# Kernel optimization log

Measured on AMD Instinct MI355X. Metric: run time of the kernel, lower is better.

## Reference

```python
import jax, jax.numpy as jnp
import numpy as np
from jax import lax

B, NS, H, L, STEPS, VOCAB, E, DOC = 8, 80, 256, 2, 8, 30000, 128, 16
NN = NS + 1


def _lstm_stack(Wx, Wh, b, carry, x):
    # flax StackedRNNCell of LSTMCells: gate order i,f,g,o; input dense (no bias) + recurrent dense (bias)
    # Wx, Wh: [L, H, 4H]; b: [L, 4H]; carry: (c, h) each [L, ..., H]; x: [..., H]
    c, h = carry
    new_c, new_h = [], []
    inp = x
    for l in range(Wx.shape[0]):
        g = inp @ Wx[l] + h[l] @ Wh[l] + b[l]
        i, f, gg, o = jnp.split(g, 4, axis=-1)
        cl = jax.nn.sigmoid(f) * c[l] + jax.nn.sigmoid(i) * jnp.tanh(gg)
        hl = jax.nn.sigmoid(o) * jnp.tanh(cl)
        new_c.append(cl)
        new_h.append(hl)
        inp = hl
    return (jnp.stack(new_c), jnp.stack(new_h)), inp


def _concat_carry(c, h):
    # tree_leaves order of [(c0,h0),(c1,h1)] is [c0,h0,c1,h1]
    parts = []
    for l in range(c.shape[0]):
        parts += [c[l], h[l]]
    return jnp.concatenate(parts, axis=-1)


def _unconcat_carry(cat, nl):
    leaves = jnp.split(cat, 2 * nl, axis=-1)
    return jnp.stack(leaves[0::2]), jnp.stack(leaves[1::2])


def _ln(x, scale, bias, eps=1e-6):
    mu = x.mean(-1, keepdims=True)
    var = ((x - mu) ** 2).mean(-1, keepdims=True)
    return (x - mu) * lax.rsqrt(var + eps) * scale + bias


def _skip_encoder(se_nh, Wx, Wh, b, ln_s, ln_b):
    # skip_emb[i, j] = LayerNormed stacked-LSTM run over statements i..j-1; shape [NN, NN, H]
    ns, hd = se_nh.shape
    nl = Wx.shape[0]
    zc = jnp.zeros((nl, hd), se_nh.dtype)

    def from_start(start):
        def f(carry, xt):
            (c, h), idx = carry
            (c2, h2), out = _lstm_stack(Wx, Wh, b, (c, h), xt)
            c2, h2 = _unconcat_carry(_ln(_concat_carry(c2, h2), ln_s, ln_b), nl)
            keep = idx >= start
            c2 = jnp.where(keep, c2, zc)
            h2 = jnp.where(keep, h2, zc)
            out = jnp.where(keep, out, jnp.zeros_like(out))
            return ((c2, h2), idx + 1), out

        _, outs = lax.scan(f, ((zc, zc), 0), se_nh)
        return jnp.concatenate([jnp.zeros((1, hd), se_nh.dtype), outs], axis=0)

    return jax.vmap(from_start)(jnp.arange(ns + 1))


def _forward(node_embeddings, st_Wx, st_Wh, st_b, sk_Wx, sk_Wh, sk_b,
             ln_scale, ln_bias, ex_Wx, ex_Wh, ex_b, wk, bk, ws, bs,
             w1, b1, wo, bo, exit_node_indexes):
    bsz, ns, hd = node_embeddings.shape
    nl = st_Wx.shape[0]
    nn_ = ns + 1
    # statement embedder: single-token (L=1) stacked-LSTM step from zero state
    z = jnp.zeros((nl, bsz, ns, hd), node_embeddings.dtype)
    _, stmt = _lstm_stack(st_Wx, st_Wh, st_b, (z, z), node_embeddings)  # [B, NS, H]
    skip = jax.vmap(lambda s: _skip_encoder(s, sk_Wx, sk_Wh, sk_b, ln_scale, ln_bias))(stmt)  # [B, NN, NN, H]
    keys = jnp.einsum('bnmh,hk->bnmk', skip, ws) + bs  # skip_dense, reused every step
    c = jnp.zeros((nl, bsz, nn_, hd), node_embeddings.dtype)
    h = jnp.zeros_like(c)
    p = jnp.zeros((bsz, nn_), node_embeddings.dtype).at[:, 0].set(1.0)
    mask_mid = (1.0 - jnp.tri(nn_)).at[:, ns].set(1.0)
    mask_init = jnp.zeros((nn_, nn_)).at[:, 1].set(1.0)
    mask_fin = jnp.zeros((nn_, nn_)).at[:, ns].set(1.0)
    for step_idx in range(STEPS):
        mask = mask_init if step_idx == 0 else (mask_fin if step_idx == STEPS - 1 else mask_mid)
        hcat = _concat_carry(c, h)  # [B, NN, 2*L*H]
        q = hcat @ wk + bk  # h_key dense -> [B, NN, H]
        logits = (jnp.tanh(q[:, :, None, :] + keys) @ w1)[..., 0] + b1[0]  # [B, NN, NN]
        logits = jnp.where(mask > 0, logits, -1e9)
        a = jax.nn.softmax(logits, axis=-1)
        t = p[:, :, None] * a  # transition mass [B, NN, NN]
        new_p = t.sum(axis=1)
        denom = new_p[:, :, None] + 1e-7
        x_in = jnp.einsum('bnm,bnmh->bmh', t, skip) / denom
        c_prop = jnp.einsum('bnm,lbnh->lbmh', t, c) / denom[None]
        h_prop = jnp.einsum('bnm,lbnh->lbmh', t, h) / denom[None]
        (c, h), _ = _lstm_stack(ex_Wx, ex_Wh, ex_b, (c_prop, h_prop), x_in)
        p = new_p
    h_exit = h[-1][jnp.arange(bsz), exit_node_indexes]  # [B, H]
    return h_exit @ wo + bo  # [B, VOCAB]


def setup_inputs():
    key = jax.random.key(0)
    ks = jax.random.split(key, 20)
    s = 1.0 / np.sqrt(H)

    def nrm(k, shape, scale):
        return jax.random.normal(k, shape, dtype=jnp.float32) * scale

    return dict(
        node_embeddings=nrm(ks[0], (B, NS, H), 1.0),
        docstring_embeddings=nrm(ks[1], (B, DOC, H), 1.0),
        docstring_mask=jnp.ones((B, DOC), dtype=bool),
        edge_sources=jax.random.randint(ks[2], (B, E), 0, NN, dtype=jnp.int32),
        edge_dests=jax.random.randint(ks[3], (B, E), 0, NN, dtype=jnp.int32),
        edge_types=jax.random.randint(ks[4], (B, E), 0, 6, dtype=jnp.int32),
        true_indexes=jax.random.randint(ks[5], (B, NS), 0, NN, dtype=jnp.int32),
        false_indexes=jax.random.randint(ks[6], (B, NS), 0, NN, dtype=jnp.int32),
        raise_indexes=jax.random.randint(ks[7], (B, NS), 0, NN, dtype=jnp.int32),
        start_node_indexes=jnp.zeros((B,), dtype=jnp.int32),
        exit_node_indexes=jnp.full((B,), NS, dtype=jnp.int32),
        step_limits=jnp.full((B,), STEPS, dtype=jnp.int32),
        st_Wx=nrm(ks[8], (L, H, 4 * H), s), st_Wh=nrm(ks[9], (L, H, 4 * H), s),
        st_b=jnp.zeros((L, 4 * H)),
        sk_Wx=nrm(ks[10], (L, H, 4 * H), s), sk_Wh=nrm(ks[11], (L, H, 4 * H), s),
        sk_b=jnp.zeros((L, 4 * H)),
        ln_scale=jnp.ones((2 * L * H,)), ln_bias=jnp.zeros((2 * L * H,)),
        ex_Wx=nrm(ks[12], (L, H, 4 * H), s), ex_Wh=nrm(ks[13], (L, H, 4 * H), s),
        ex_b=jnp.zeros((L, 4 * H)),
        wk=nrm(ks[14], (2 * L * H, H), 1.0 / np.sqrt(2 * L * H)), bk=jnp.zeros((H,)),
        ws=nrm(ks[15], (H, H), s), bs=jnp.zeros((H,)),
        w1=nrm(ks[16], (H, 1), s), b1=jnp.zeros((1,)),
        wo=nrm(ks[17], (H, VOCAB), s), bo=jnp.zeros((VOCAB,)),
    )


def reference(node_embeddings, docstring_embeddings, docstring_mask, edge_sources,
              edge_dests, edge_types, true_indexes, false_indexes, raise_indexes,
              start_node_indexes, exit_node_indexes, step_limits,
              st_Wx, st_Wh, st_b, sk_Wx, sk_Wh, sk_b, ln_scale, ln_bias,
              ex_Wx, ex_Wh, ex_b, wk, bk, ws, bs, w1, b1, wo, bo):
    # docstring_* and edge index args are accepted per the model signature but are
    # not used in the visible forward body.
    return _forward(node_embeddings, st_Wx, st_Wh, st_b, sk_Wx, sk_Wh, sk_b,
                    ln_scale, ln_bias, ex_Wx, ex_Wh, ex_b, wk, bk, ws, bs,
                    w1, b1, wo, bo, exit_node_indexes)
```

## Files before the change

kernel.cpp:

```cpp
#include <hip/hip_runtime.h>

typedef unsigned int  u32;
typedef unsigned short u16;
typedef float v2f __attribute__((ext_vector_type(2)));
typedef __attribute__((ext_vector_type(8))) short bfv8;
typedef __attribute__((ext_vector_type(4))) float f32x4;

#define ROWS 648

__device__ __forceinline__ float sigf(float x){ return 1.0f/(1.0f+__expf(-x)); }
__device__ __forceinline__ float tanh_fast(float x){
  float e = __expf(-2.0f*fabsf(x));
  float r = (1.0f-e)/(1.0f+e);
  return copysignf(r,x);
}
__device__ __forceinline__ u16 f2bf(float f){
  u32 u = __float_as_uint(f);
  u += 0x7FFFu + ((u>>16)&1u);
  return (u16)(u>>16);
}
__device__ __forceinline__ u32 packbf2(float lo, float hi){
  return (u32)f2bf(lo) | ((u32)f2bf(hi)<<16);
}
__device__ __forceinline__ float bf2f(u16 v){ return __uint_as_float(((u32)v)<<16); }
__device__ __forceinline__ float bflo(u32 u){ return __uint_as_float(u<<16); }
__device__ __forceinline__ float bfhi(u32 u){ return __uint_as_float(u & 0xFFFF0000u); }
__device__ __forceinline__ v2f unpk(u32 w){
  v2f r; r.x = bflo(w); r.y = bfhi(w); return r;
}

__global__ void pack_pairs(const float* __restrict__ src, u32* __restrict__ dst,
                           int Kpairs, int ncol){
  int id = blockIdx.x*256 + threadIdx.x;
  if (id >= Kpairs*ncol) return;
  int k2 = id / ncol, j = id - k2*ncol;
  dst[id] = packbf2(src[(2*k2)*ncol + j], src[(2*k2+1)*ncol + j]);
}

__global__ void pack_mfma(const float* __restrict__ A, const float* __restrict__ Bm,
                          u32* __restrict__ dst, int K){
  int id = blockIdx.x*256 + threadIdx.x;
  int KS = K >> 5;
  int tot = 64*KS*64*4;
  if (id >= tot) return;
  int e2 = id & 3;
  int l  = (id >> 2) & 63;
  int rest = id >> 8;
  int ks = rest % KS;
  int t  = rest / KS;
  int k  = ks*32 + (l>>4)*8 + e2*2;
  int col = t*16 + (l&15);
  float v0 = (k   < 256) ? A[k*1024 + col]       : Bm[(k-256)*1024 + col];
  float v1 = (k+1 < 256) ? A[(k+1)*1024 + col]   : Bm[(k+1-256)*1024 + col];
  dst[id] = packbf2(v0, v1);
}

__global__ void k_init_p(float* __restrict__ p0){
  int i = blockIdx.x*256 + threadIdx.x;
  if (i < ROWS) p0[i] = ((i % 81)==0) ? 1.0f : 0.0f;
}

__global__ __launch_bounds__(512) void k_stmt_x0(
    const float* __restrict__ ne, const float* __restrict__ stWx, const float* __restrict__ stb,
    const float* __restrict__ skWx, const float* __restrict__ skb, float4* __restrict__ X0){
  __shared__ float xv[2][256];
  __shared__ float hv[2][256];
  int r = threadIdx.x >> 8, j = threadIdx.x & 255;
  int bn = blockIdx.x*2 + r;
  xv[r][j] = ne[bn*256 + j];
  __syncthreads();
  float a0=stb[j], a2=stb[512+j], a3=stb[768+j];
  for (int k=0;k<256;k++){
    float x = xv[r][k];
    const float* w = stWx + k*1024;
    a0 = fmaf(x, w[j], a0); a2 = fmaf(x, w[512+j], a2); a3 = fmaf(x, w[768+j], a3);
  }
  float c = sigf(a0)*tanh_fast(a2);
  float h = sigf(a3)*tanh_fast(c);
  hv[r][j] = h;
  __syncthreads();
  a0=stb[1024+j]; a2=stb[1536+j]; a3=stb[1792+j];
  const float* W1 = stWx + 256*1024;
  for (int k=0;k<256;k++){
    float x = hv[r][k];
    const float* w = W1 + k*1024;
    a0 = fmaf(x, w[j], a0); a2 = fmaf(x, w[512+j], a2); a3 = fmaf(x, w[768+j], a3);
  }
  c = sigf(a0)*tanh_fast(a2);
  h = sigf(a3)*tanh_fast(c);
  __syncthreads();
  xv[r][j] = h;
  __syncthreads();
  float b0=skb[j], b1g=skb[256+j], b2=skb[512+j], b3=skb[768+j];
  for (int k=0;k<256;k++){
    float x = xv[r][k];
    const float* w = skWx + k*1024;
    b0 = fmaf(x, w[j], b0);     b1g = fmaf(x, w[256+j], b1g);
    b2 = fmaf(x, w[512+j], b2); b3 = fmaf(x, w[768+j], b3);
  }
  X0[bn*256 + j] = make_float4(b0,b1g,b2,b3);
}

#define RS0 264
#define RS1 520
__global__ __launch_bounds__(1024) void k_skip_chains(
    const float4* __restrict__ X0,
    const uint4* __restrict__ W0m, const uint4* __restrict__ W1m,
    const float* __restrict__ skb, const float* __restrict__ lnS, const float* __restrict__ lnB,
    float* __restrict__ skip){
  int s  = blockIdx.x;
  int tid = threadIdx.x;
  int w = tid >> 6, lane = tid & 63;
  int l15 = lane & 15, l4 = lane >> 4;
  int rp = tid >> 8, j = tid & 255;
  __shared__ float part[8*1024];
  __shared__ u16 A0h[16*RS0], A0l[16*RS0];
  __shared__ u16 A1h[16*RS1], A1l[16*RS1];
  __shared__ float red[4][16];
  for (int i=tid; i<16*RS0; i+=1024){ A0h[i]=0; A0l[i]=0; }
  for (int i=tid; i<16*RS1; i+=1024){ A1h[i]=0; A1l[i]=0; }
  float c0a=0.f, c1a=0.f, c0b=0.f, c1b=0.f;
  float s1b0=skb[1024+j], s1b1=skb[1280+j], s1b2=skb[1536+j], s1b3=skb[1792+j];
  float lS0=lnS[j], lS1=lnS[256+j], lS2=lnS[512+j], lS3=lnS[768+j];
  float lB0=lnB[j], lB1=lnB[256+j], lB2=lnB[512+j], lB3=lnB[768+j];
  const int aoff0 = l15*RS0 + l4*8;
  const int aoff1 = l15*RS1 + l4*8;
  __syncthreads();
  for (int idx=s; idx<80; idx++){
    float4 gxa = X0[(rp*80+idx)*256 + j];
    float4 gxb = X0[((rp+4)*80+idx)*256 + j];
    f32x4 acc0={0,0,0,0}, acc1={0,0,0,0}, acc2={0,0,0,0}, acc3={0,0,0,0};
    #pragma unroll 4
    for (int ks=0; ks<8; ks++){
      bfv8 ah = *(const bfv8*)&A0h[aoff0 + ks*32];
      bfv8 al = *(const bfv8*)&A0l[aoff0 + ks*32];
      uint4 b0 = W0m[((w*4+0)*8 + ks)*64 + lane];
      uint4 b1 = W0m[((w*4+1)*8 + ks)*64 + lane];
      uint4 b2 = W0m[((w*4+2)*8 + ks)*64 + lane];
      uint4 b3 = W0m[((w*4+3)*8 + ks)*64 + lane];
      bfv8 v0=__builtin_bit_cast(bfv8,b0), v1=__builtin_bit_cast(bfv8,b1);
      bfv8 v2=__builtin_bit_cast(bfv8,b2), v3=__builtin_bit_cast(bfv8,b3);
      acc0=__builtin_amdgcn_mfma_f32_16x16x32_bf16(ah,v0,acc0,0,0,0);
      acc0=__builtin_amdgcn_mfma_f32_16x16x32_bf16(al,v0,acc0,0,0,0);
      acc1=__builtin_amdgcn_mfma_f32_16x16x32_bf16(ah,v1,acc1,0,0,0);
      acc1=__builtin_amdgcn_mfma_f32_16x16x32_bf16(al,v1,acc1,0,0,0);
      acc2=__builtin_amdgcn_mfma_f32_16x16x32_bf16(ah,v2,acc2,0,0,0);
      acc2=__builtin_amdgcn_mfma_f32_16x16x32_bf16(al,v2,acc2,0,0,0);
      acc3=__builtin_amdgcn_mfma_f32_16x16x32_bf16(ah,v3,acc3,0,0,0);
      acc3=__builtin_amdgcn_mfma_f32_16x16x32_bf16(al,v3,acc3,0,0,0);
    }
    if (lane < 32){
      int r0 = l4*4;
      #pragma unroll
      for (int q=0;q<4;q++){
        part[(r0+q)*1024 + w*64 +  0 + l15] = acc0[q];
        part[(r0+q)*1024 + w*64 + 16 + l15] = acc1[q];
        part[(r0+q)*1024 + w*64 + 32 + l15] = acc2[q];
        part[(r0+q)*1024 + w*64 + 48 + l15] = acc3[q];
      }
    }
    __syncthreads();
    float h0na, h0nb;
    {
      float a0=gxa.x+part[rp*1024+j],     a1=gxa.y+part[rp*1024+256+j];
      float a2=gxa.z+part[rp*1024+512+j], a3=gxa.w+part[rp*1024+768+j];
      float ii=sigf(a0), ff=sigf(a1), gg=tanh_fast(a2), oo=sigf(a3);
      c0a = ff*c0a + ii*gg;
      h0na = oo*tanh_fast(c0a);
      u16 hi = f2bf(h0na);
      A1h[rp*RS1 + j] = hi;
      A1l[rp*RS1 + j] = f2bf(h0na - bf2f(hi));
    }
    {
      int rb = rp+4;
      float a0=gxb.x+part[rb*1024+j],     a1=gxb.y+part[rb*1024+256+j];
      float a2=gxb.z+part[rb*1024+512+j], a3=gxb.w+part[rb*1024+768+j];
      float ii=sigf(a0), ff=sigf(a1), gg=tanh_fast(a2), oo=sigf(a3);
      c0b = ff*c0b + ii*gg;
      h0nb = oo*tanh_fast(c0b);
      u16 hi = f2bf(h0nb);
      A1h[rb*RS1 + j] = hi;
      A1l[rb*RS1 + j] = f2bf(h0nb - bf2f(hi));
    }
    __syncthreads();
    acc0=(f32x4){0,0,0,0}; acc1=(f32x4){0,0,0,0}; acc2=(f32x4){0,0,0,0}; acc3=(f32x4){0,0,0,0};
    #pragma unroll 4
    for (int ks=0; ks<16; ks++){
      bfv8 ah = *(const bfv8*)&A1h[aoff1 + ks*32];
      bfv8 al = *(const bfv8*)&A1l[aoff1 + ks*32];
      uint4 b0 = W1m[((w*4+0)*16 + ks)*64 + lane];
      uint4 b1 = W1m[((w*4+1)*16 + ks)*64 + lane];
      uint4 b2 = W1m[((w*4+2)*16 + ks)*64 + lane];
      uint4 b3 = W1m[((w*4+3)*16 + ks)*64 + lane];
      bfv8 v0=__builtin_bit_cast(bfv8,b0), v1=__builtin_bit_cast(bfv8,b1);
      bfv8 v2=__builtin_bit_cast(bfv8,b2), v3=__builtin_bit_cast(bfv8,b3);
      acc0=__builtin_amdgcn_mfma_f32_16x16x32_bf16(ah,v0,acc0,0,0,0);
      acc0=__builtin_amdgcn_mfma_f32_16x16x32_bf16(al,v0,acc0,0,0,0);
      acc1=__builtin_amdgcn_mfma_f32_16x16x32_bf16(ah,v1,acc1,0,0,0);
      acc1=__builtin_amdgcn_mfma_f32_16x16x32_bf16(al,v1,acc1,0,0,0);
      acc2=__builtin_amdgcn_mfma_f32_16x16x32_bf16(ah,v2,acc2,0,0,0);
      acc2=__builtin_amdgcn_mfma_f32_16x16x32_bf16(al,v2,acc2,0,0,0);
      acc3=__builtin_amdgcn_mfma_f32_16x16x32_bf16(ah,v3,acc3,0,0,0);
      acc3=__builtin_amdgcn_mfma_f32_16x16x32_bf16(al,v3,acc3,0,0,0);
    }
    if (lane < 32){
      int r0 = l4*4;
      #pragma unroll
      for (int q=0;q<4;q++){
        part[(r0+q)*1024 + w*64 +  0 + l15] = acc0[q];
        part[(r0+q)*1024 + w*64 + 16 + l15] = acc1[q];
        part[(r0+q)*1024 + w*64 + 32 + l15] = acc2[q];
        part[(r0+q)*1024 + w*64 + 48 + l15] = acc3[q];
      }
    }
    __syncthreads();
    float h1na, h1nb;
    {
      float a0=s1b0+part[rp*1024+j],     a1=s1b1+part[rp*1024+256+j];
      float a2=s1b2+part[rp*1024+512+j], a3=s1b3+part[rp*1024+768+j];
      float ii=sigf(a0), ff=sigf(a1), gg=tanh_fast(a2), oo=sigf(a3);
      c1a = ff*c1a + ii*gg;
      h1na = oo*tanh_fast(c1a);
      skip[((rp*81 + s)*81 + (idx+1))*256 + j] = h1na;
    }
    {
      int rb = rp+4;
      float a0=s1b0+part[rb*1024+j],     a1=s1b1+part[rb*1024+256+j];
      float a2=s1b2+part[rb*1024+512+j], a3=s1b3+part[rb*1024+768+j];
      float ii=sigf(a0), ff=sigf(a1), gg=tanh_fast(a2), oo=sigf(a3);
      c1b = ff*c1b + ii*gg;
      h1nb = oo*tanh_fast(c1b);
      skip[((rb*81 + s)*81 + (idx+1))*256 + j] = h1nb;
    }
    float sm0 = c0a + h0na + c1a + h1na;
    float sq0 = c0a*c0a + h0na*h0na + c1a*c1a + h1na*h1na;
    float sm1 = c0b + h0nb + c1b + h1nb;
    float sq1 = c0b*c0b + h0nb*h0nb + c1b*c1b + h1nb*h1nb;
    #pragma unroll
    for (int off=32; off; off>>=1){
      sm0 += __shfl_xor(sm0, off); sq0 += __shfl_xor(sq0, off);
      sm1 += __shfl_xor(sm1, off); sq1 += __shfl_xor(sq1, off);
    }
    int wq = j >> 6;
    if ((j & 63) == 0){
      red[rp][wq*4+0]=sm0; red[rp][wq*4+1]=sq0;
      red[rp][wq*4+2]=sm1; red[rp][wq*4+3]=sq1;
    }
    __syncthreads();
    sm0 = red[rp][0]+red[rp][4]+red[rp][8]+red[rp][12];
    sq0 = red[rp][1]+red[rp][5]+red[rp][9]+red[rp][13];
    sm1 = red[rp][2]+red[rp][6]+red[rp][10]+red[rp][14];
    sq1 = red[rp][3]+red[rp][7]+red[rp][11]+red[rp][15];
    {
      float mu = sm0 * (1.0f/1024.0f);
      float var = sq0 * (1.0f/1024.0f) - mu*mu;
      float rstd = rsqrtf(var + 1e-6f);
      c0a = (c0a - mu)*rstd*lS0 + lB0;
      float h0ln = (h0na - mu)*rstd*lS1 + lB1;
      c1a = (c1a - mu)*rstd*lS2 + lB2;
      float h1ln = (h1na - mu)*rstd*lS3 + lB3;
      u16 hi = f2bf(h0ln);
      A0h[rp*RS0 + j] = hi; A0l[rp*RS0 + j] = f2bf(h0ln - bf2f(hi));
      hi = f2bf(h1ln);
      A1h[rp*RS1 + 256 + j] = hi; A1l[rp*RS1 + 256 + j] = f2bf(h1ln - bf2f(hi));
    }
    {
      int rb = rp+4;
      float mu = sm1 * (1.0f/1024.0f);
      float var = sq1 * (1.0f/1024.0f) - mu*mu;
      float rstd = rsqrtf(var + 1e-6f);
      c0b = (c0b - mu)*rstd*lS0 + lB0;
      float h0ln = (h0nb - mu)*rstd*lS1 + lB1;
      c1b = (c1b - mu)*rstd*lS2 + lB2;
      float h1ln = (h1nb - mu)*rstd*lS3 + lB3;
      u16 hi = f2bf(h0ln);
      A0h[rb*RS0 + j] = hi; A0l[rb*RS0 + j] = f2bf(h0ln - bf2f(hi));
      hi = f2bf(h1ln);
      A1h[rb*RS1 + 256 + j] = hi; A1l[rb*RS1 + 256 + j] = f2bf(h1ln - bf2f(hi));
    }
    __syncthreads();
  }
}

__global__ __launch_bounds__(256) void k_keys(const float* __restrict__ skip,
    const u32* __restrict__ wspk, const float* __restrict__ bs, u16* __restrict__ keys){
  __shared__ float skr[8][256];
  int tid = threadIdx.x;
  int bn = blockIdx.x;
  float bsv = bs[tid];
  const float4* sk4 = (const float4*)skip;
  for (int m0=0; m0<81; m0+=8){
    int mc = (81-m0 < 8) ? (81-m0) : 8;
    for (int i=tid; i<mc*64; i+=256){
      int mm = i>>6, kk = i&63;
      float4 v = sk4[(bn*81 + m0 + mm)*64 + kk];
      skr[mm][4*kk+0]=v.x; skr[mm][4*kk+1]=v.y; skr[mm][4*kk+2]=v.z; skr[mm][4*kk+3]=v.w;
    }
    __syncthreads();
    v2f acc[8];
    #pragma unroll
    for (int qq=0;qq<8;qq++) acc[qq]=(v2f){0.f,0.f};
    for (int k2=0;k2<128;k2++){
      v2f w2 = unpk(wspk[k2*256+tid]);
      #pragma unroll
      for (int qq=0;qq<8;qq++){
        v2f sv = *(const v2f*)&skr[qq][2*k2];
        acc[qq] += sv*w2;
      }
    }
    for (int qq=0;qq<mc;qq++) keys[(bn*81+m0+qq)*256+tid] = f2bf(acc[qq].x+acc[qq].y+bsv);
    __syncthreads();
  }
}

__global__ __launch_bounds__(256) void k_attn(
    const float* __restrict__ c0g, const float* __restrict__ h0g,
    const float* __restrict__ c1g, const float* __restrict__ h1g,
    const u32* __restrict__ wkp, const float* __restrict__ bk,
    const u16* __restrict__ keys, const float* __restrict__ w1,
    const float* __restrict__ pcur, float* __restrict__ t, int mode){
  int bn = blockIdx.x; int n = bn % 81;
  int tid = threadIdx.x;
  float pv = pcur[bn];
  if (pv == 0.0f){
    if (tid < 81) t[bn*81 + tid] = 0.0f;
    return;
  }
  __shared__ float hc[1024];
  __shared__ float qv[256];
  __shared__ float lg[81];
  hc[tid]      = c0g[bn*256+tid];
  hc[256+tid]  = h0g[bn*256+tid];
  hc[512+tid]  = c1g[bn*256+tid];
  hc[768+tid]  = h1g[bn*256+tid];
  if (tid < 81) lg[tid] = -3e38f;
  __syncthreads();
  v2f A = {bk[tid], 0.f};
  #pragma unroll 8
  for (int k2=0;k2<512;k2++){
    v2f hp = *(const v2f*)&hc[2*k2];
    A += hp*unpk(wkp[k2*256+tid]);
  }
  qv[tid] = A.x + A.y;
  __syncthreads();
  int lane = tid & 63, wv = tid >> 6;
  float w1v0 = w1[lane], w1v1 = w1[64+lane], w1v2 = w1[128+lane], w1v3 = w1[192+lane];
  for (int m = wv; m < 81; m += 4){
    bool um = (mode==0) ? (m==1) : (mode==2) ? (m==80) : (m>n || m==80);
    if (!um) continue;
    const u16* kr = keys + (bn*81+m)*256;
    float acc;
    acc  = tanh_fast(qv[lane]     + bf2f(kr[lane]))     * w1v0;
    acc += tanh_fast(qv[64+lane]  + bf2f(kr[64+lane]))  * w1v1;
    acc += tanh_fast(qv[128+lane] + bf2f(kr[128+lane])) * w1v2;
    acc += tanh_fast(qv[192+lane] + bf2f(kr[192+lane])) * w1v3;
    #pragma unroll
    for (int off=32; off; off>>=1) acc += __shfl_xor(acc, off);
    if (lane==0) lg[m] = acc;
  }
  __syncthreads();
  if (tid < 64){
    float v1 = lg[tid];
    float v2 = (tid<17) ? lg[64+tid] : -3e38f;
    float mx = fmaxf(v1, v2);
    #pragma unroll
    for (int off=32; off; off>>=1) mx = fmaxf(mx, __shfl_xor(mx, off));
    float e1 = __expf(v1-mx);
    float e2 = (tid<17) ? __expf(v2-mx) : 0.0f;
    float ssum = e1+e2;
    #pragma unroll
    for (int off=32; off; off>>=1) ssum += __shfl_xor(ssum, off);
    float sc = pv / ssum;
    t[bn*81 + tid] = e1*sc;
    if (tid<17) t[bn*81 + 64+tid] = e2*sc;
  }
}

__global__ __launch_bounds__(256) void k_gather(
    const float* __restrict__ t, const float* __restrict__ skip,
    const float* __restrict__ c0i, const float* __restrict__ h0i,
    const float* __restrict__ c1i, const float* __restrict__ h1i,
    float* __restrict__ xin, float* __restrict__ h0p,
    float* __restrict__ h1p, float* __restrict__ c0p,
    float* __restrict__ c1p, float* __restrict__ pnext){
  int row = blockIdx.x;
  int b = row / 81, m = row - b*81;
  int tid = threadIdx.x;
  __shared__ float tcol[81];
  if (tid < 81) tcol[tid] = t[(b*81+tid)*81 + m];
  __syncthreads();
  int nlim = (m==80) ? 81 : m;
  float ts = 0.f;
  for (int n=0;n<nlim;n++) ts += tcol[n];
  if (tid==0) pnext[row] = ts;
  int o = row*256 + tid;
  if (ts == 0.0f){
    xin[o]=0.f; h0p[o]=0.f; h1p[o]=0.f; c0p[o]=0.f; c1p[o]=0.f;
    return;
  }
  float xa=0.f, c0a=0.f, h0a=0.f, c1a=0.f, h1a=0.f;
  for (int n=0;n<nlim;n++){
    float tv = tcol[n];
    int st = (b*81+n)*256 + tid;
    xa  = fmaf(tv, skip[((b*81+n)*81 + m)*256 + tid], xa);
    c0a = fmaf(tv, c0i[st], c0a);
    h0a = fmaf(tv, h0i[st], h0a);
    c1a = fmaf(tv, c1i[st], c1a);
    h1a = fmaf(tv, h1i[st], h1a);
  }
  float inv = 1.0f/(ts + 1e-7f);
  xin[o]=xa*inv; h0p[o]=h0a*inv; h1p[o]=h1a*inv; c0p[o]=c0a*inv; c1p[o]=c1a*inv;
}

#define RSX 520
__global__ __launch_bounds__(1024) void k_exlstm(
    const float* __restrict__ xin, const float* __restrict__ h0pg,
    const float* __restrict__ h1pg, const float* __restrict__ c0pg,
    const float* __restrict__ c1pg,
    const uint4* __restrict__ WAm, const uint4* __restrict__ WBm,
    const float* __restrict__ exb,
    float* __restrict__ c0o, float* __restrict__ h0o,
    float* __restrict__ c1o, float* __restrict__ h1o){
  int row0 = blockIdx.x*16;
  int tid = threadIdx.x;
  int w = tid >> 6, lane = tid & 63;
  int l15 = lane & 15, l4 = lane >> 4;
  int rp = tid >> 8, j = tid & 255;
  __shared__ float part[16*1024];
  __shared__ u16 Ah[16*RSX], Al[16*RSX];
  {
    int r16 = w, c4 = lane;
    int grow = row0 + r16;
    float4 vx = {0,0,0,0}, vh = {0,0,0,0};
    if (grow < ROWS){
      vx = ((const float4*)xin)[grow*64 + c4];
      vh = ((const float4*)h0pg)[grow*64 + c4];
    }
    ushort4 hi4, lo4;
    hi4.x=f2bf(vx.x); lo4.x=f2bf(vx.x-bf2f(hi4.x));
    hi4.y=f2bf(vx.y); lo4.y=f2bf(vx.y-bf2f(hi4.y));
    hi4.z=f2bf(vx.z); lo4.z=f2bf(vx.z-bf2f(hi4.z));
    hi4.w=f2bf(vx.w); lo4.w=f2bf(vx.w-bf2f(hi4.w));
    *(ushort4*)&Ah[r16*RSX + c4*4] = hi4;
    *(ushort4*)&Al[r16*RSX + c4*4] = lo4;
    hi4.x=f2bf(vh.x); lo4.x=f2bf(vh.x-bf2f(hi4.x));
    hi4.y=f2bf(vh.y); lo4.y=f2bf(vh.y-bf2f(hi4.y));
    hi4.z=f2bf(vh.z); lo4.z=f2bf(vh.z-bf2f(hi4.z));
    hi4.w=f2bf(vh.w); lo4.w=f2bf(vh.w-bf2f(hi4.w));
    *(ushort4*)&Ah[r16*RSX + 256 + c4*4] = hi4;
    *(ushort4*)&Al[r16*RSX + 256 + c4*4] = lo4;
  }
  __syncthreads();
  const int aoff = l15*RSX + l4*8;
  f32x4 acc0={0,0,0,0}, acc1={0,0,0,0}, acc2={0,0,0,0}, acc3={0,0,0,0};
  #pragma unroll 4
  for (int ks=0; ks<16; ks++){
    bfv8 ah = *(const bfv8*)&Ah[aoff + ks*32];
    bfv8 al = *(const bfv8*)&Al[aoff + ks*32];
    uint4 b0 = WAm[((w*4+0)*16 + ks)*64 + lane];
    uint4 b1 = WAm[((w*4+1)*16 + ks)*64 + lane];
    uint4 b2 = WAm[((w*4+2)*16 + ks)*64 + lane];
    uint4 b3 = WAm[((w*4+3)*16 + ks)*64 + lane];
    bfv8 v0=__builtin_bit_cast(bfv8,b0), v1=__builtin_bit_cast(bfv8,b1);
    bfv8 v2=__builtin_bit_cast(bfv8,b2), v3=__builtin_bit_cast(bfv8,b3);
    acc0=__builtin_amdgcn_mfma_f32_16x16x32_bf16(ah,v0,acc0,0,0,0);
    acc0=__builtin_amdgcn_mfma_f32_16x16x32_bf16(al,v0,acc0,0,0,0);
    acc1=__builtin_amdgcn_mfma_f32_16x16x32_bf16(ah,v1,acc1,0,0,0);
    acc1=__builtin_amdgcn_mfma_f32_16x16x32_bf16(al,v1,acc1,0,0,0);
    acc2=__builtin_amdgcn_mfma_f32_16x16x32_bf16(ah,v2,acc2,0,0,0);
    acc2=__builtin_amdgcn_mfma_f32_16x16x32_bf16(al,v2,acc2,0,0,0);
    acc3=__builtin_amdgcn_mfma_f32_16x16x32_bf16(ah,v3,acc3,0,0,0);
    acc3=__builtin_amdgcn_mfma_f32_16x16x32_bf16(al,v3,acc3,0,0,0);
  }
  {
    int r0 = l4*4;
    #pragma unroll
    for (int q=0;q<4;q++){
      part[(r0+q)*1024 + w*64 +  0 + l15] = acc0[q];
      part[(r0+q)*1024 + w*64 + 16 + l15] = acc1[q];
      part[(r0+q)*1024 + w*64 + 32 + l15] = acc2[q];
      part[(r0+q)*1024 + w*64 + 48 + l15] = acc3[q];
    }
  }
  __syncthreads();
  float eb0=exb[j], eb1=exb[256+j], eb2=exb[512+j], eb3=exb[768+j];
  float c0s[4], h0s[4];
  #pragma unroll
  for (int q=0;q<4;q++){
    int r = 4*q + rp;
    int grow = row0 + r;
    bool g = grow < ROWS;
    float a0 = eb0 + part[r*1024 + j];
    float a1 = eb1 + part[r*1024 + 256 + j];
    float a2 = eb2 + part[r*1024 + 512 + j];
    float a3 = eb3 + part[r*1024 + 768 + j];
    float cp = g ? c0pg[grow*256 + j] : 0.f;
    float ii=sigf(a0), ff=sigf(a1), gg=tanh_fast(a2), oo=sigf(a3);
    float cn = ff*cp + ii*gg;
    float hn = oo*tanh_fast(cn);
    c0s[q]=cn; h0s[q]=hn;
    u16 hi = f2bf(hn);
    Ah[r*RSX + j] = hi; Al[r*RSX + j] = f2bf(hn - bf2f(hi));
    float hp = g ? h1pg[grow*256 + j] : 0.f;
    hi = f2bf(hp);
    Ah[r*RSX + 256 + j] = hi; Al[r*RSX + 256 + j] = f2bf(hp - bf2f(hi));
  }
  __syncthreads();
  acc0=(f32x4){0,0,0,0}; acc1=(f32x4){0,0,0,0}; acc2=(f32x4){0,0,0,0}; acc3=(f32x4){0,0,0,0};
  #pragma unroll 4
  for (int ks=0; ks<16; ks++){
    bfv8 ah = *(const bfv8*)&Ah[aoff + ks*32];
    bfv8 al = *(const bfv8*)&Al[aoff + ks*32];
    uint4 b0 = WBm[((w*4+0)*16 + ks)*64 + lane];
    uint4 b1 = WBm[((w*4+1)*16 + ks)*64 + lane];
    uint4 b2 = WBm[((w*4+2)*16 + ks)*64 + lane];
    uint4 b3 = WBm[((w*4+3)*16 + ks)*64 + lane];
    bfv8 v0=__builtin_bit_cast(bfv8,b0), v1=__builtin_bit_cast(bfv8,b1);
    bfv8 v2=__builtin_bit_cast(bfv8,b2), v3=__builtin_bit_cast(bfv8,b3);
    acc0=__builtin_amdgcn_mfma_f32_16x16x32_bf16(ah,v0,acc0,0,0,0);
    acc0=__builtin_amdgcn_mfma_f32_16x16x32_bf16(al,v0,acc0,0,0,0);
    acc1=__builtin_amdgcn_mfma_f32_16x16x32_bf16(ah,v1,acc1,0,0,0);
    acc1=__builtin_amdgcn_mfma_f32_16x16x32_bf16(al,v1,acc1,0,0,0);
    acc2=__builtin_amdgcn_mfma_f32_16x16x32_bf16(ah,v2,acc2,0,0,0);
    acc2=__builtin_amdgcn_mfma_f32_16x16x32_bf16(al,v2,acc2,0,0,0);
    acc3=__builtin_amdgcn_mfma_f32_16x16x32_bf16(ah,v3,acc3,0,0,0);
    acc3=__builtin_amdgcn_mfma_f32_16x16x32_bf16(al,v3,acc3,0,0,0);
  }
  {
    int r0 = l4*4;
    #pragma unroll
    for (int q=0;q<4;q++){
      part[(r0+q)*1024 + w*64 +  0 + l15] = acc0[q];
      part[(r0+q)*1024 + w*64 + 16 + l15] = acc1[q];
      part[(r0+q)*1024 + w*64 + 32 + l15] = acc2[q];
      part[(r0+q)*1024 + w*64 + 48 + l15] = acc3[q];
    }
  }
  __syncthreads();
  float eb4=exb[1024+j], eb5=exb[1280+j], eb6=exb[1536+j], eb7=exb[1792+j];
  #pragma unroll
  for (int q=0;q<4;q++){
    int r = 4*q + rp;
    int grow = row0 + r;
    bool g = grow < ROWS;
    float a0 = eb4 + part[r*1024 + j];
    float a1 = eb5 + part[r*1024 + 256 + j];
    float a2 = eb6 + part[r*1024 + 512 + j];
    float a3 = eb7 + part[r*1024 + 768 + j];
    float cp = g ? c1pg[grow*256 + j] : 0.f;
    float ii=sigf(a0), ff=sigf(a1), gg=tanh_fast(a2), oo=sigf(a3);
    float cn = ff*cp + ii*gg;
    float hn = oo*tanh_fast(cn);
    if (g){
      int o = grow*256 + j;
      c0o[o]=c0s[q]; h0o[o]=h0s[q]; c1o[o]=cn; h1o[o]=hn;
    }
  }
}

__global__ __launch_bounds__(256) void k_out(
    const float* __restrict__ h1f, const int* __restrict__ exitIdx,
    const float* __restrict__ wo, const float* __restrict__ bo, float* __restrict__ out){
  __shared__ float hv[8][256];
  int tid = threadIdx.x;
  for (int i = tid; i < 2048; i += 256){
    int b = i >> 8, k = i & 255;
    hv[b][k] = h1f[(b*81 + exitIdx[b])*256 + k];
  }
  __syncthreads();
  int v = blockIdx.x*256 + tid;
  if (v >= 30000) return;
  float acc[8];
  #pragma unroll
  for (int b=0;b<8;b++) acc[b] = bo[v];
  for (int k=0;k<256;k++){
    float w = wo[k*30000 + v];
    #pragma unroll
    for (int b=0;b<8;b++) acc[b] = fmaf(hv[b][k], w, acc[b]);
  }
  #pragma unroll
  for (int b=0;b<8;b++) out[b*30000+v] = acc[b];
}

extern "C" void kernel_launch(void* const* d_in, const int* in_sizes, int n_in,
                              void* d_out, int out_size, void* d_ws, size_t ws_size,
                              hipStream_t stream){
  (void)in_sizes; (void)n_in; (void)out_size;
  const float* ne    = (const float*)d_in[0];
  const int*   exitI = (const int*)d_in[10];
  const float* stWx  = (const float*)d_in[12];
  const float* stb   = (const float*)d_in[14];
  const float* skWx  = (const float*)d_in[15];
  const float* skWh  = (const float*)d_in[16];
  const float* skb   = (const float*)d_in[17];
  const float* lnS   = (const float*)d_in[18];
  const float* lnB   = (const float*)d_in[19];
  const float* exWx  = (const float*)d_in[20];
  const float* exWh  = (const float*)d_in[21];
  const float* exb   = (const float*)d_in[22];
  const float* wk    = (const float*)d_in[23];
  const float* bk    = (const float*)d_in[24];
  const float* wsm   = (const float*)d_in[25];
  const float* bs    = (const float*)d_in[26];
  const float* w1    = (const float*)d_in[27];
  const float* wo    = (const float*)d_in[29];
  const float* bo    = (const float*)d_in[30];
  float* out = (float*)d_out;

  char* w = (char*)d_ws;
  size_t off = 0;
  auto alloc = [&](size_t bytes)->char*{
    char* p = w + off; off += (bytes + 255) & ~size_t(255); return p;
  };
  float4* X0   = (float4*)alloc((size_t)640*256*16);
  u32* W0m     = (u32*)alloc((size_t)131072*4);
  u32* W1m     = (u32*)alloc((size_t)262144*4);
  u32* WAm     = (u32*)alloc((size_t)262144*4);
  u32* WBm     = (u32*)alloc((size_t)262144*4);
  u32* wkp     = (u32*)alloc((size_t)512*256*4);
  u32* wspk    = (u32*)alloc((size_t)128*256*4);
  float* skip  = (float*)alloc((size_t)8*81*81*256*4);
  u16* keys    = (u16*)alloc((size_t)8*81*81*256*2);
  float* tb    = (float*)alloc((size_t)ROWS*81*4);
  float* p0    = (float*)alloc(ROWS*4);
  float* p1    = (float*)alloc(ROWS*4);
  float* stA   = (float*)alloc((size_t)4*ROWS*256*4);
  float* stB   = (float*)alloc((size_t)4*ROWS*256*4);
  float* xinb  = (float*)alloc((size_t)ROWS*256*4);
  float* h0pb  = (float*)alloc((size_t)ROWS*256*4);
  float* h1pb  = (float*)alloc((size_t)ROWS*256*4);
  float* c0pb  = (float*)alloc((size_t)ROWS*256*4);
  float* c1pb  = (float*)alloc((size_t)ROWS*256*4);
  if (off > ws_size) return;

  const size_t ST = (size_t)ROWS*256;
  float *A_c0=stA, *A_h0=stA+ST, *A_c1=stA+2*ST, *A_h1=stA+3*ST;
  float *B_c0=stB, *B_h0=stB+ST, *B_c1=stB+2*ST, *B_h1=stB+3*ST;

  hipMemsetAsync(skip, 0, (size_t)8*81*81*256*4, stream);
  hipMemsetAsync(stA, 0, (size_t)4*ROWS*256*4, stream);
  hipMemsetAsync(stB, 0, (size_t)4*ROWS*256*4, stream);
  k_init_p<<<3,256,0,stream>>>(p0);

  pack_mfma<<<512, 256, 0, stream>>>(skWh, skWh, W0m, 256);
  pack_mfma<<<1024,256, 0, stream>>>(skWx+256*1024, skWh+256*1024, W1m, 512);
  pack_mfma<<<1024,256, 0, stream>>>(exWx, exWh, WAm, 512);
  pack_mfma<<<1024,256, 0, stream>>>(exWx+256*1024, exWh+256*1024, WBm, 512);
  pack_pairs<<<512, 256, 0, stream>>>(wk, wkp, 512, 256);
  pack_pairs<<<128, 256, 0, stream>>>(wsm, wspk, 128, 256);

  k_stmt_x0<<<320, 512, 0, stream>>>(ne, stWx, stb, skWx, skb, X0);
  k_skip_chains<<<80, 1024, 0, stream>>>(X0, (const uint4*)W0m, (const uint4*)W1m,
                                         skb, lnS, lnB, skip);
  k_keys<<<648, 256, 0, stream>>>(skip, wspk, bs, keys);

  float* pc = p0; float* pn = p1;
  for (int s=0; s<8; s++){
    float *ic0,*ih0,*ic1,*ih1,*oc0,*oh0,*oc1,*oh1;
    if ((s & 1) == 0){ ic0=A_c0; ih0=A_h0; ic1=A_c1; ih1=A_h1; oc0=B_c0; oh0=B_h0; oc1=B_c1; oh1=B_h1; }
    else             { ic0=B_c0; ih0=B_h0; ic1=B_c1; ih1=B_h1; oc0=A_c0; oh0=A_h0; oc1=A_c1; oh1=A_h1; }
    int mode = (s==0) ? 0 : ((s==7) ? 2 : 1);
    k_attn<<<648, 256, 0, stream>>>(ic0, ih0, ic1, ih1, wkp, bk, keys, w1, pc, tb, mode);
    k_gather<<<648, 256, 0, stream>>>(tb, skip, ic0, ih0, ic1, ih1,
                                      xinb, h0pb, h1pb, c0pb, c1pb, pn);
    k_exlstm<<<41, 1024, 0, stream>>>(xinb, h0pb, h1pb, c0pb, c1pb,
                                      (const uint4*)WAm, (const uint4*)WBm, exb,
                                      oc0, oh0, oc1, oh1);
    float* tmp = pc; pc = pn; pn = tmp;
  }
  k_out<<<(30000+255)/256, 256, 0, stream>>>(A_h1, exitI, wo, bo, out);
}
```

Measured before the change: 2.267 ms.

## Move key and query projections to split-bf16 MFMA and fuse query into exit LSTM

The skip-embedding key projection changes from a scalar packed-bf16 loop to MFMA tiles of 16 rows, using hi/lo bf16 splitting to keep fp32-like accuracy. The per-step query projection (carry times wk) moves out of k_attn into the tail of k_exlstm, where the new carry is already in registers and can be staged in LDS for MFMA. k_attn now reads the precomputed query, and its mode 0 and mode 2 steps exit early with a one-hot result. Shared partial buffers are padded to reduce LDS bank conflicts. The cost is extra LDS and a third MFMA phase in k_exlstm, which runs on only 41 blocks.

```diff
diff --git a/kernel.cpp b/kernel.cpp
--- a/kernel.cpp
+++ b/kernel.cpp
@@ -7,6 +7,7 @@
 typedef __attribute__((ext_vector_type(4))) float f32x4;
 
 #define ROWS 648
+#define KROWS 52488
 
 __device__ __forceinline__ float sigf(float x){ return 1.0f/(1.0f+__expf(-x)); }
 __device__ __forceinline__ float tanh_fast(float x){
@@ -23,19 +24,6 @@
   return (u32)f2bf(lo) | ((u32)f2bf(hi)<<16);
 }
 __device__ __forceinline__ float bf2f(u16 v){ return __uint_as_float(((u32)v)<<16); }
-__device__ __forceinline__ float bflo(u32 u){ return __uint_as_float(u<<16); }
-__device__ __forceinline__ float bfhi(u32 u){ return __uint_as_float(u & 0xFFFF0000u); }
-__device__ __forceinline__ v2f unpk(u32 w){
-  v2f r; r.x = bflo(w); r.y = bfhi(w); return r;
-}
-
-__global__ void pack_pairs(const float* __restrict__ src, u32* __restrict__ dst,
-                           int Kpairs, int ncol){
-  int id = blockIdx.x*256 + threadIdx.x;
-  if (id >= Kpairs*ncol) return;
-  int k2 = id / ncol, j = id - k2*ncol;
-  dst[id] = packbf2(src[(2*k2)*ncol + j], src[(2*k2+1)*ncol + j]);
-}
 
 __global__ void pack_mfma(const float* __restrict__ A, const float* __restrict__ Bm,
                           u32* __restrict__ dst, int K){
@@ -55,6 +43,23 @@
   dst[id] = packbf2(v0, v1);
 }
 
+__global__ void pack_w(const float* __restrict__ src, u32* __restrict__ dst,
+                       int K, int NT){
+  int id = blockIdx.x*256 + threadIdx.x;
+  int KS = K >> 5;
+  int tot = NT*KS*64*4;
+  if (id >= tot) return;
+  int e2 = id & 3;
+  int l  = (id >> 2) & 63;
+  int rest = id >> 8;
+  int ks = rest % KS;
+  int t  = rest / KS;
+  int k  = ks*32 + (l>>4)*8 + e2*2;
+  int col = t*16 + (l&15);
+  int ld = NT*16;
+  dst[id] = packbf2(src[k*ld + col], src[(k+1)*ld + col]);
+}
+
 __global__ void k_init_p(float* __restrict__ p0){
   int i = blockIdx.x*256 + threadIdx.x;
   if (i < ROWS) p0[i] = ((i % 81)==0) ? 1.0f : 0.0f;
@@ -103,6 +108,7 @@
 
 #define RS0 264
 #define RS1 520
+#define PS  1028
 __global__ __launch_bounds__(1024) void k_skip_chains(
     const float4* __restrict__ X0,
     const uint4* __restrict__ W0m, const uint4* __restrict__ W1m,
@@ -113,7 +119,7 @@
   int w = tid >> 6, lane = tid & 63;
   int l15 = lane & 15, l4 = lane >> 4;
   int rp = tid >> 8, j = tid & 255;
-  __shared__ float part[8*1024];
+  __shared__ float part[8*PS];
   __shared__ u16 A0h[16*RS0], A0l[16*RS0];
   __shared__ u16 A1h[16*RS1], A1l[16*RS1];
   __shared__ float red[4][16];
@@ -153,17 +159,17 @@
       int r0 = l4*4;
       #pragma unroll
       for (int q=0;q<4;q++){
-        part[(r0+q)*1024 + w*64 +  0 + l15] = acc0[q];
-        part[(r0+q)*1024 + w*64 + 16 + l15] = acc1[q];
-        part[(r0+q)*1024 + w*64 + 32 + l15] = acc2[q];
-        part[(r0+q)*1024 + w*64 + 48 + l15] = acc3[q];
+        part[(r0+q)*PS + w*64 +  0 + l15] = acc0[q];
+        part[(r0+q)*PS + w*64 + 16 + l15] = acc1[q];
+        part[(r0+q)*PS + w*64 + 32 + l15] = acc2[q];
+        part[(r0+q)*PS + w*64 + 48 + l15] = acc3[q];
       }
     }
     __syncthreads();
     float h0na, h0nb;
     {
-      float a0=gxa.x+part[rp*1024+j],     a1=gxa.y+part[rp*1024+256+j];
-      float a2=gxa.z+part[rp*1024+512+j], a3=gxa.w+part[rp*1024+768+j];
+      float a0=gxa.x+part[rp*PS+j],     a1=gxa.y+part[rp*PS+256+j];
+      float a2=gxa.z+part[rp*PS+512+j], a3=gxa.w+part[rp*PS+768+j];
       float ii=sigf(a0), ff=sigf(a1), gg=tanh_fast(a2), oo=sigf(a3);
       c0a = ff*c0a + ii*gg;
       h0na = oo*tanh_fast(c0a);
@@ -173,8 +179,8 @@
     }
     {
       int rb = rp+4;
-      float a0=gxb.x+part[rb*1024+j],     a1=gxb.y+part[rb*1024+256+j];
-      float a2=gxb.z+part[rb*1024+512+j], a3=gxb.w+part[rb*1024+768+j];
+      float a0=gxb.x+part[rb*PS+j],     a1=gxb.y+part[rb*PS+256+j];
+      float a2=gxb.z+part[rb*PS+512+j], a3=gxb.w+part[rb*PS+768+j];
       float ii=sigf(a0), ff=sigf(a1), gg=tanh_fast(a2), oo=sigf(a3);
       c0b = ff*c0b + ii*gg;
       h0nb = oo*tanh_fast(c0b);
@@ -207,17 +213,17 @@
       int r0 = l4*4;
       #pragma unroll
       for (int q=0;q<4;q++){
-        part[(r0+q)*1024 + w*64 +  0 + l15] = acc0[q];
-        part[(r0+q)*1024 + w*64 + 16 + l15] = acc1[q];
-        part[(r0+q)*1024 + w*64 + 32 + l15] = acc2[q];
-        part[(r0+q)*1024 + w*64 + 48 + l15] = acc3[q];
+        part[(r0+q)*PS + w*64 +  0 + l15] = acc0[q];
+        part[(r0+q)*PS + w*64 + 16 + l15] = acc1[q];
+        part[(r0+q)*PS + w*64 + 32 + l15] = acc2[q];
+        part[(r0+q)*PS + w*64 + 48 + l15] = acc3[q];
       }
     }
     __syncthreads();
     float h1na, h1nb;
     {
-      float a0=s1b0+part[rp*1024+j],     a1=s1b1+part[rp*1024+256+j];
-      float a2=s1b2+part[rp*1024+512+j], a3=s1b3+part[rp*1024+768+j];
+      float a0=s1b0+part[rp*PS+j],     a1=s1b1+part[rp*PS+256+j];
+      float a2=s1b2+part[rp*PS+512+j], a3=s1b3+part[rp*PS+768+j];
       float ii=sigf(a0), ff=sigf(a1), gg=tanh_fast(a2), oo=sigf(a3);
       c1a = ff*c1a + ii*gg;
       h1na = oo*tanh_fast(c1a);
@@ -225,8 +231,8 @@
     }
     {
       int rb = rp+4;
-      float a0=s1b0+part[rb*1024+j],     a1=s1b1+part[rb*1024+256+j];
-      float a2=s1b2+part[rb*1024+512+j], a3=s1b3+part[rb*1024+768+j];
+      float a0=s1b0+part[rb*PS+j],     a1=s1b1+part[rb*PS+256+j];
+      float a2=s1b2+part[rb*PS+512+j], a3=s1b3+part[rb*PS+768+j];
       float ii=sigf(a0), ff=sigf(a1), gg=tanh_fast(a2), oo=sigf(a3);
       c1b = ff*c1b + ii*gg;
       h1nb = oo*tanh_fast(c1b);
@@ -282,43 +288,54 @@
   }
 }
 
-__global__ __launch_bounds__(256) void k_keys(const float* __restrict__ skip,
-    const u32* __restrict__ wspk, const float* __restrict__ bs, u16* __restrict__ keys){
-  __shared__ float skr[8][256];
+__global__ __launch_bounds__(1024) void k_keys(const float* __restrict__ skip,
+    const uint4* __restrict__ WSm, const float* __restrict__ bs, u16* __restrict__ keys){
+  int rows0 = blockIdx.x*16;
   int tid = threadIdx.x;
-  int bn = blockIdx.x;
-  float bsv = bs[tid];
-  const float4* sk4 = (const float4*)skip;
-  for (int m0=0; m0<81; m0+=8){
-    int mc = (81-m0 < 8) ? (81-m0) : 8;
-    for (int i=tid; i<mc*64; i+=256){
-      int mm = i>>6, kk = i&63;
-      float4 v = sk4[(bn*81 + m0 + mm)*64 + kk];
-      skr[mm][4*kk+0]=v.x; skr[mm][4*kk+1]=v.y; skr[mm][4*kk+2]=v.z; skr[mm][4*kk+3]=v.w;
-    }
-    __syncthreads();
-    v2f acc[8];
-    #pragma unroll
-    for (int qq=0;qq<8;qq++) acc[qq]=(v2f){0.f,0.f};
-    for (int k2=0;k2<128;k2++){
-      v2f w2 = unpk(wspk[k2*256+tid]);
-      #pragma unroll
-      for (int qq=0;qq<8;qq++){
-        v2f sv = *(const v2f*)&skr[qq][2*k2];
-        acc[qq] += sv*w2;
-      }
-    }
-    for (int qq=0;qq<mc;qq++) keys[(bn*81+m0+qq)*256+tid] = f2bf(acc[qq].x+acc[qq].y+bsv);
-    __syncthreads();
-  }
+  int w = tid >> 6, lane = tid & 63;
+  int l15 = lane & 15, l4 = lane >> 4;
+  __shared__ u16 Ah[16*RS0], Al[16*RS0];
+  __shared__ u16 kbuf[16*256];
+  {
+    int grow = rows0 + w;
+    float4 v = {0,0,0,0};
+    if (grow < KROWS) v = ((const float4*)skip)[grow*64 + lane];
+    ushort4 hi4, lo4;
+    hi4.x=f2bf(v.x); lo4.x=f2bf(v.x-bf2f(hi4.x));
+    hi4.y=f2bf(v.y); lo4.y=f2bf(v.y-bf2f(hi4.y));
+    hi4.z=f2bf(v.z); lo4.z=f2bf(v.z-bf2f(hi4.z));
+    hi4.w=f2bf(v.w); lo4.w=f2bf(v.w-bf2f(hi4.w));
+    *(ushort4*)&Ah[w*RS0 + lane*4] = hi4;
+    *(ushort4*)&Al[w*RS0 + lane*4] = lo4;
+  }
+  __syncthreads();
+  const int aoff = l15*RS0 + l4*8;
+  f32x4 acc = {0,0,0,0};
+  #pragma unroll
+  for (int ks=0; ks<8; ks++){
+    bfv8 ah = *(const bfv8*)&Ah[aoff + ks*32];
+    bfv8 al = *(const bfv8*)&Al[aoff + ks*32];
+    uint4 b = WSm[(w*8 + ks)*64 + lane];
+    bfv8 v = __builtin_bit_cast(bfv8, b);
+    acc = __builtin_amdgcn_mfma_f32_16x16x32_bf16(ah, v, acc, 0,0,0);
+    acc = __builtin_amdgcn_mfma_f32_16x16x32_bf16(al, v, acc, 0,0,0);
+  }
+  float bsv = bs[w*16 + l15];
+  #pragma unroll
+  for (int q=0;q<4;q++)
+    kbuf[(l4*4+q)*256 + w*16 + l15] = f2bf(acc[q] + bsv);
+  __syncthreads();
+  int nval = KROWS - rows0; if (nval > 16) nval = 16;
+  int words = nval*128;
+  u32* kout = (u32*)keys + (size_t)rows0*128;
+  const u32* kin = (const u32*)kbuf;
+  for (int i=tid; i<words; i+=1024) kout[i] = kin[i];
 }
 
 __global__ __launch_bounds__(256) void k_attn(
-    const float* __restrict__ c0g, const float* __restrict__ h0g,
-    const float* __restrict__ c1g, const float* __restrict__ h1g,
-    const u32* __restrict__ wkp, const float* __restrict__ bk,
-    const u16* __restrict__ keys, const float* __restrict__ w1,
-    const float* __restrict__ pcur, float* __restrict__ t, int mode){
+    const float* __restrict__ qb, const u16* __restrict__ keys,
+    const float* __restrict__ w1, const float* __restrict__ pcur,
+    float* __restrict__ t, int mode){
   int bn = blockIdx.x; int n = bn % 81;
   int tid = threadIdx.x;
   float pv = pcur[bn];
@@ -326,28 +343,17 @@
     if (tid < 81) t[bn*81 + tid] = 0.0f;
     return;
   }
-  __shared__ float hc[1024];
+  if (mode == 0){ if (tid < 81) t[bn*81 + tid] = (tid==1)  ? pv : 0.0f; return; }
+  if (mode == 2){ if (tid < 81) t[bn*81 + tid] = (tid==80) ? pv : 0.0f; return; }
   __shared__ float qv[256];
   __shared__ float lg[81];
-  hc[tid]      = c0g[bn*256+tid];
-  hc[256+tid]  = h0g[bn*256+tid];
-  hc[512+tid]  = c1g[bn*256+tid];
-  hc[768+tid]  = h1g[bn*256+tid];
+  qv[tid] = qb[bn*256 + tid];
   if (tid < 81) lg[tid] = -3e38f;
-  __syncthreads();
-  v2f A = {bk[tid], 0.f};
-  #pragma unroll 8
-  for (int k2=0;k2<512;k2++){
-    v2f hp = *(const v2f*)&hc[2*k2];
-    A += hp*unpk(wkp[k2*256+tid]);
-  }
-  qv[tid] = A.x + A.y;
   __syncthreads();
   int lane = tid & 63, wv = tid >> 6;
   float w1v0 = w1[lane], w1v1 = w1[64+lane], w1v2 = w1[128+lane], w1v3 = w1[192+lane];
   for (int m = wv; m < 81; m += 4){
-    bool um = (mode==0) ? (m==1) : (mode==2) ? (m==80) : (m>n || m==80);
-    if (!um) continue;
+    if (!(m>n || m==80)) continue;
     const u16* kr = keys + (bn*81+m)*256;
     float acc;
     acc  = tanh_fast(qv[lane]     + bf2f(kr[lane]))     * w1v0;
@@ -412,43 +418,45 @@
   xin[o]=xa*inv; h0p[o]=h0a*inv; h1p[o]=h1a*inv; c0p[o]=c0a*inv; c1p[o]=c1a*inv;
 }
 
-#define RSX 520
+#define RSX 1032
+#define PSX 1028
 __global__ __launch_bounds__(1024) void k_exlstm(
     const float* __restrict__ xin, const float* __restrict__ h0pg,
     const float* __restrict__ h1pg, const float* __restrict__ c0pg,
     const float* __restrict__ c1pg,
     const uint4* __restrict__ WAm, const uint4* __restrict__ WBm,
-    const float* __restrict__ exb,
+    const uint4* __restrict__ WKm,
+    const float* __restrict__ exb, const float* __restrict__ bk,
     float* __restrict__ c0o, float* __restrict__ h0o,
-    float* __restrict__ c1o, float* __restrict__ h1o){
+    float* __restrict__ c1o, float* __restrict__ h1o,
+    float* __restrict__ qb){
   int row0 = blockIdx.x*16;
   int tid = threadIdx.x;
   int w = tid >> 6, lane = tid & 63;
   int l15 = lane & 15, l4 = lane >> 4;
   int rp = tid >> 8, j = tid & 255;
-  __shared__ float part[16*1024];
+  __shared__ float part[16*PSX];
   __shared__ u16 Ah[16*RSX], Al[16*RSX];
   {
-    int r16 = w, c4 = lane;
-    int grow = row0 + r16;
+    int grow = row0 + w;
     float4 vx = {0,0,0,0}, vh = {0,0,0,0};
     if (grow < ROWS){
-      vx = ((const float4*)xin)[grow*64 + c4];
-      vh = ((const float4*)h0pg)[grow*64 + c4];
+      vx = ((const float4*)xin)[grow*64 + lane];
+      vh = ((const float4*)h0pg)[grow*64 + lane];
     }
     ushort4 hi4, lo4;
     hi4.x=f2bf(vx.x); lo4.x=f2bf(vx.x-bf2f(hi4.x));
     hi4.y=f2bf(vx.y); lo4.y=f2bf(vx.y-bf2f(hi4.y));
     hi4.z=f2bf(vx.z); lo4.z=f2bf(vx.z-bf2f(hi4.z));
     hi4.w=f2bf(vx.w); lo4.w=f2bf(vx.w-bf2f(hi4.w));
-    *(ushort4*)&Ah[r16*RSX + c4*4] = hi4;
-    *(ushort4*)&Al[r16*RSX + c4*4] = lo4;
+    *(ushort4*)&Ah[w*RSX + lane*4] = hi4;
+    *(ushort4*)&Al[w*RSX + lane*4] = lo4;
     hi4.x=f2bf(vh.x); lo4.x=f2bf(vh.x-bf2f(hi4.x));
     hi4.y=f2bf(vh.y); lo4.y=f2bf(vh.y-bf2f(hi4.y));
     hi4.z=f2bf(vh.z); lo4.z=f2bf(vh.z-bf2f(hi4.z));
     hi4.w=f2bf(vh.w); lo4.w=f2bf(vh.w-bf2f(hi4.w));
-    *(ushort4*)&Ah[r16*RSX + 256 + c4*4] = hi4;
-    *(ushort4*)&Al[r16*RSX + 256 + c4*4] = lo4;
+    *(ushort4*)&Ah[w*RSX + 256 + lane*4] = hi4;
+    *(ushort4*)&Al[w*RSX + 256 + lane*4] = lo4;
   }
   __syncthreads();
   const int aoff = l15*RSX + l4*8;
@@ -476,10 +484,10 @@
     int r0 = l4*4;
     #pragma unroll
     for (int q=0;q<4;q++){
-      part[(r0+q)*1024 + w*64 +  0 + l15] = acc0[q];
-      part[(r0+q)*1024 + w*64 + 16 + l15] = acc1[q];
-      part[(r0+q)*1024 + w*64 + 32 + l15] = acc2[q];
-      part[(r0+q)*1024 + w*64 + 48 + l15] = acc3[q];
+      part[(r0+q)*PSX + w*64 +  0 + l15] = acc0[q];
+      part[(r0+q)*PSX + w*64 + 16 + l15] = acc1[q];
+      part[(r0+q)*PSX + w*64 + 32 + l15] = acc2[q];
+      part[(r0+q)*PSX + w*64 + 48 + l15] = acc3[q];
     }
   }
   __syncthreads();
@@ -490,10 +498,10 @@
     int r = 4*q + rp;
     int grow = row0 + r;
     bool g = grow < ROWS;
-    float a0 = eb0 + part[r*1024 + j];
-    float a1 = eb1 + part[r*1024 + 256 + j];
-    float a2 = eb2 + part[r*1024 + 512 + j];
-    float a3 = eb3 + part[r*1024 + 768 + j];
+    float a0 = eb0 + part[r*PSX + j];
+    float a1 = eb1 + part[r*PSX + 256 + j];
+    float a2 = eb2 + part[r*PSX + 512 + j];
+    float a3 = eb3 + part[r*PSX + 768 + j];
     float cp = g ? c0pg[grow*256 + j] : 0.f;
     float ii=sigf(a0), ff=sigf(a1), gg=tanh_fast(a2), oo=sigf(a3);
     float cn = ff*cp + ii*gg;
@@ -530,10 +538,10 @@
     int r0 = l4*4;
     #pragma unroll
     for (int q=0;q<4;q++){
-      part[(r0+q)*1024 + w*64 +  0 + l15] = acc0[q];
-      part[(r0+q)*1024 + w*64 + 16 + l15] = acc1[q];
-      part[(r0+q)*1024 + w*64 + 32 + l15] = acc2[q];
-      part[(r0+q)*1024 + w*64 + 48 + l15] = acc3[q];
+      part[(r0+q)*PSX + w*64 +  0 + l15] = acc0[q];
+      part[(r0+q)*PSX + w*64 + 16 + l15] = acc1[q];
+      part[(r0+q)*PSX + w*64 + 32 + l15] = acc2[q];
+      part[(r0+q)*PSX + w*64 + 48 + l15] = acc3[q];
     }
   }
   __syncthreads();
@@ -543,10 +551,10 @@
     int r = 4*q + rp;
     int grow = row0 + r;
     bool g = grow < ROWS;
-    float a0 = eb4 + part[r*1024 + j];
-    float a1 = eb5 + part[r*1024 + 256 + j];
-    float a2 = eb6 + part[r*1024 + 512 + j];
-    float a3 = eb7 + part[r*1024 + 768 + j];
+    float a0 = eb4 + part[r*PSX + j];
+    float a1 = eb5 + part[r*PSX + 256 + j];
+    float a2 = eb6 + part[r*PSX + 512 + j];
+    float a3 = eb7 + part[r*PSX + 768 + j];
     float cp = g ? c1pg[grow*256 + j] : 0.f;
     float ii=sigf(a0), ff=sigf(a1), gg=tanh_fast(a2), oo=sigf(a3);
     float cn = ff*cp + ii*gg;
@@ -555,6 +563,36 @@
       int o = grow*256 + j;
       c0o[o]=c0s[q]; h0o[o]=h0s[q]; c1o[o]=cn; h1o[o]=hn;
     }
+    u16 hi;
+    hi = f2bf(c0s[q]); Ah[r*RSX +       j] = hi; Al[r*RSX +       j] = f2bf(c0s[q]-bf2f(hi));
+    hi = f2bf(h0s[q]); Ah[r*RSX + 256 + j] = hi; Al[r*RSX + 256 + j] = f2bf(h0s[q]-bf2f(hi));
+    hi = f2bf(cn);     Ah[r*RSX + 512 + j] = hi; Al[r*RSX + 512 + j] = f2bf(cn-bf2f(hi));
+    hi = f2bf(hn);     Ah[r*RSX + 768 + j] = hi; Al[r*RSX + 768 + j] = f2bf(hn-bf2f(hi));
+  }
+  __syncthreads();
+  f32x4 accq = {0,0,0,0};
+  #pragma unroll 4
+  for (int ks=0; ks<32; ks++){
+    bfv8 ah = *(const bfv8*)&Ah[aoff + ks*32];
+    bfv8 al = *(const bfv8*)&Al[aoff + ks*32];
+    uint4 b = WKm[(w*32 + ks)*64 + lane];
+    bfv8 v = __builtin_bit_cast(bfv8, b);
+    accq = __builtin_amdgcn_mfma_f32_16x16x32_bf16(ah, v, accq, 0,0,0);
+    accq = __builtin_amdgcn_mfma_f32_16x16x32_bf16(al, v, accq, 0,0,0);
+  }
+  {
+    int r0 = l4*4;
+    #pragma unroll
+    for (int q=0;q<4;q++)
+      part[(r0+q)*260 + w*16 + l15] = accq[q];
+  }
+  __syncthreads();
+  float bkv = bk[j];
+  #pragma unroll
+  for (int q=0;q<4;q++){
+    int r = 4*q + rp;
+    int grow = row0 + r;
+    if (grow < ROWS) qb[grow*256 + j] = part[r*260 + j] + bkv;
   }
 }
 
@@ -617,8 +655,8 @@
   u32* W1m     = (u32*)alloc((size_t)262144*4);
   u32* WAm     = (u32*)alloc((size_t)262144*4);
   u32* WBm     = (u32*)alloc((size_t)262144*4);
-  u32* wkp     = (u32*)alloc((size_t)512*256*4);
-  u32* wspk    = (u32*)alloc((size_t)128*256*4);
+  u32* WKm     = (u32*)alloc((size_t)131072*4);
+  u32* WSm     = (u32*)alloc((size_t)32768*4);
   float* skip  = (float*)alloc((size_t)8*81*81*256*4);
   u16* keys    = (u16*)alloc((size_t)8*81*81*256*2);
   float* tb    = (float*)alloc((size_t)ROWS*81*4);
@@ -631,6 +669,7 @@
   float* h1pb  = (float*)alloc((size_t)ROWS*256*4);
   float* c0pb  = (float*)alloc((size_t)ROWS*256*4);
   float* c1pb  = (float*)alloc((size_t)ROWS*256*4);
+  float* qb    = (float*)alloc((size_t)ROWS*256*4);
   if (off > ws_size) return;
 
   const size_t ST = (size_t)ROWS*256;
@@ -646,13 +685,13 @@
   pack_mfma<<<1024,256, 0, stream>>>(skWx+256*1024, skWh+256*1024, W1m, 512);
   pack_mfma<<<1024,256, 0, stream>>>(exWx, exWh, WAm, 512);
   pack_mfma<<<1024,256, 0, stream>>>(exWx+256*1024, exWh+256*1024, WBm, 512);
-  pack_pairs<<<512, 256, 0, stream>>>(wk, wkp, 512, 256);
-  pack_pairs<<<128, 256, 0, stream>>>(wsm, wspk, 128, 256);
+  pack_w<<<512, 256, 0, stream>>>(wk, WKm, 1024, 16);
+  pack_w<<<128, 256, 0, stream>>>(wsm, WSm, 256, 16);
 
   k_stmt_x0<<<320, 512, 0, stream>>>(ne, stWx, stb, skWx, skb, X0);
   k_skip_chains<<<80, 1024, 0, stream>>>(X0, (const uint4*)W0m, (const uint4*)W1m,
                                          skb, lnS, lnB, skip);
-  k_keys<<<648, 256, 0, stream>>>(skip, wspk, bs, keys);
+  k_keys<<<(KROWS+15)/16, 1024, 0, stream>>>(skip, (const uint4*)WSm, bs, keys);
 
   float* pc = p0; float* pn = p1;
   for (int s=0; s<8; s++){
@@ -660,12 +699,13 @@
     if ((s & 1) == 0){ ic0=A_c0; ih0=A_h0; ic1=A_c1; ih1=A_h1; oc0=B_c0; oh0=B_h0; oc1=B_c1; oh1=B_h1; }
     else             { ic0=B_c0; ih0=B_h0; ic1=B_c1; ih1=B_h1; oc0=A_c0; oh0=A_h0; oc1=A_c1; oh1=A_h1; }
     int mode = (s==0) ? 0 : ((s==7) ? 2 : 1);
-    k_attn<<<648, 256, 0, stream>>>(ic0, ih0, ic1, ih1, wkp, bk, keys, w1, pc, tb, mode);
+    k_attn<<<648, 256, 0, stream>>>(qb, keys, w1, pc, tb, mode);
     k_gather<<<648, 256, 0, stream>>>(tb, skip, ic0, ih0, ic1, ih1,
                                       xinb, h0pb, h1pb, c0pb, c1pb, pn);
     k_exlstm<<<41, 1024, 0, stream>>>(xinb, h0pb, h1pb, c0pb, c1pb,
-                                      (const uint4*)WAm, (const uint4*)WBm, exb,
-                                      oc0, oh0, oc1, oh1);
+                                      (const uint4*)WAm, (const uint4*)WBm,
+                                      (const uint4*)WKm, exb, bk,
+                                      oc0, oh0, oc1, oh1, qb);
     float* tmp = pc; pc = pn; pn = tmp;
   }
   k_out<<<(30000+255)/256, 256, 0, stream>>>(A_h1, exitI, wo, bo, out);
```

New measurement: 2.024 ms, median of 2. 1.12x faster.
